# Kernel optimization log

Hardware: AMD Instinct MI355X
Metric: run time of the kernel (lower is better)

The kernel has to match this reference:

```python
import jax, jax.numpy as jnp
import numpy as np

B, T, H, CH = 8192, 10, 512, 512  # batch, time_step, hidden_size, code_hidden_size (must be equal)


def setup_inputs() -> dict:
    key = jax.random.key(0)
    ks = jax.random.split(key, 18)
    s = 0.05
    inp = {
        "h": jax.random.normal(ks[0], (B, T, CH), dtype=jnp.float32),
        "y_seq": jax.random.normal(ks[1], (B, T), dtype=jnp.float32),
        "attn1_w": jax.random.normal(ks[2], (CH, 2 * H), dtype=jnp.float32) * s,
        "attn1_b": jax.random.normal(ks[3], (CH,), dtype=jnp.float32) * s,
        "attn2_w": jax.random.normal(ks[4], (CH, CH), dtype=jnp.float32) * s,
        "attn2_b": jax.random.normal(ks[5], (CH,), dtype=jnp.float32) * s,
        "attn3_w": jax.random.normal(ks[6], (1, CH), dtype=jnp.float32) * s,
        "attn3_b": jax.random.normal(ks[7], (1,), dtype=jnp.float32) * s,
        "W_ih": jax.random.normal(ks[8], (4 * H, 1), dtype=jnp.float32) * s,
        "W_hh": jax.random.normal(ks[9], (4 * H, H), dtype=jnp.float32) * s,
        "b_ih": jax.random.normal(ks[10], (4 * H,), dtype=jnp.float32) * s,
        "b_hh": jax.random.normal(ks[11], (4 * H,), dtype=jnp.float32) * s,
        "fc1_w": jax.random.normal(ks[12], (H, CH + H), dtype=jnp.float32) * s,
        "fc1_b": jax.random.normal(ks[13], (H,), dtype=jnp.float32) * s,
        "fc2_w": jax.random.normal(ks[14], (1, H), dtype=jnp.float32) * s,
        "fc2_b": jax.random.normal(ks[15], (1,), dtype=jnp.float32) * s,
    }
    return inp


def reference(h, y_seq, attn1_w, attn1_b, attn2_w, attn2_b, attn3_w, attn3_b,
              W_ih, W_hh, b_ih, b_hh, fc1_w, fc1_b, fc2_w, fc2_b):
    # h: [B, T, CH] -> scan over time; y_seq: [B, T]
    h_t = jnp.transpose(h, (1, 0, 2))      # [T, B, CH]
    y_t = jnp.transpose(y_seq, (1, 0))     # [T, B]
    b = h.shape[0]
    hid = W_hh.shape[1]
    d0 = jnp.zeros((b, hid), dtype=h.dtype)
    s0 = jnp.zeros((b, hid), dtype=h.dtype)

    def step(carry, xs):
        d, s = carry
        ht, yt = xs  # ht: [B, CH], yt: [B]
        # attention scores (note: original softmax is over a singleton dim -> weights == 1)
        x = jnp.concatenate([d, ht], axis=1)                       # [B, 2H]
        a = jnp.tanh((x @ attn1_w.T + attn1_b) @ attn2_w.T + attn2_b)
        w = a @ attn3_w.T + attn3_b                                # [B, 1]
        w = jax.nn.softmax(w, axis=1)                              # softmax over size-1 dim == 1
        h1 = w * ht                                                # [B, H] (CH == H)
        # single LSTM step with h0 = h1, c0 = s, input = yt (scalar feature)
        gates = yt[:, None] @ W_ih.T + b_ih + h1 @ W_hh.T + b_hh   # [B, 4H]
        i, f, g, o = jnp.split(gates, 4, axis=1)
        c = jax.nn.sigmoid(f) * s + jax.nn.sigmoid(i) * jnp.tanh(g)
        d_new = jax.nn.sigmoid(o) * jnp.tanh(c)
        return (d_new, c), None

    (d, s), _ = jax.lax.scan(step, (d0, s0), (h_t, y_t))
    z = jnp.concatenate([d, h_t[-1]], axis=1)                      # [B, CH+H]
    y_res = (z @ fc1_w.T + fc1_b) @ fc2_w.T + fc2_b                # [B, 1]
    return y_res
```

## Files before the change

### kernel.cpp

```cpp
#include <hip/hip_runtime.h>
#include <stdint.h>

typedef __attribute__((ext_vector_type(8))) short short8;
typedef __attribute__((ext_vector_type(4))) float f32x4;
typedef unsigned short ushort_t;

#define T_STEPS 10
#define BT 128
#define WPACK_BYTES (2048*1024)
#define VBUF_OFF  WPACK_BYTES
#define HBF_OFF   (WPACK_BYTES + 8192)
#define H_ELEMS   (8192ull*T_STEPS*512)
#define HBF_BYTES (H_ELEMS*2)

typedef const __attribute__((address_space(1))) void gas_void;
typedef __attribute__((address_space(3))) void las_void;

__device__ __forceinline__ void gld_lds16(const void* g, void* l){
  __builtin_amdgcn_global_load_lds((gas_void*)g, (las_void*)l, 16, 0, 0);
}

__device__ __forceinline__ unsigned int pk2(float x, float y){
  unsigned int bx = __float_as_uint(x), by = __float_as_uint(y);
  bx = (bx + 0x7FFFu + ((bx>>16)&1u)) >> 16;
  by = (by + 0x7FFFu + ((by>>16)&1u)) >> 16;
  return bx | (by<<16);
}
__device__ __forceinline__ float sigf(float x){ return 1.f/(1.f + __expf(-x)); }
__device__ __forceinline__ float tanh_(float x){
  x = fminf(fmaxf(x, -15.f), 15.f);
  float e = __expf(2.f*x);
  return (e - 1.f)/(e + 1.f);
}

__global__ __launch_bounds__(256) void k_pack(const float* __restrict__ Whh,
                                              ushort_t* __restrict__ wp){
  int id  = blockIdx.x*256 + threadIdx.x;
  int row = id >> 6;
  int ko  = (id & 63) * 8;
  const float* p = Whh + row*512 + ko;
  float4 a = *(const float4*)p, b = *(const float4*)(p+4);
  uint4 v;
  v.x = pk2(a.x,a.y); v.y = pk2(a.z,a.w);
  v.z = pk2(b.x,b.y); v.w = pk2(b.z,b.w);
  int g = row >> 9, j = row & 511;
  int jb = j >> 6, jt = (j >> 4) & 3, jl = j & 15;
  int kc = ko >> 5, khi = (ko >> 3) & 3, lane = khi*16 + jl;
  int chunk = ((jb*4 + jt)*4 + g)*16 + kc;
  *(uint4*)(wp + chunk*512 + lane*8) = v;
}

__global__ __launch_bounds__(256) void k_v(const float* __restrict__ fc1w,
                                           const float* __restrict__ fc1b,
                                           const float* __restrict__ fc2w,
                                           const float* __restrict__ fc2b,
                                           float* __restrict__ vout,
                                           float* __restrict__ bias0){
  __shared__ float red[4][64];
  int tid = threadIdx.x;
  if (blockIdx.x < 16){
    int j  = blockIdx.x*64 + (tid & 63);
    int hc = tid >> 6;
    float s = 0.f;
    for (int hh = hc*128; hh < hc*128 + 128; ++hh)
      s += fc2w[hh] * fc1w[hh*1024 + j];
    red[hc][tid & 63] = s;
    __syncthreads();
    if (tid < 64)
      vout[blockIdx.x*64 + tid] = red[0][tid]+red[1][tid]+red[2][tid]+red[3][tid];
  } else {
    if (tid < 64){
      float s = 0.f;
      for (int i = 0; i < 8; ++i){ int hh = i*64 + tid; s += fc2w[hh]*fc1b[hh]; }
      for (int m = 32; m; m >>= 1) s += __shfl_xor(s, m);
      if (tid == 0) *bias0 = s + fc2b[0];
    }
  }
}

__global__ __launch_bounds__(512) void k_init(const float* __restrict__ h,
                                              const float* __restrict__ v,
                                              const float* __restrict__ bias0,
                                              float* __restrict__ out){
  int w = threadIdx.x >> 6, lane = threadIdx.x & 63;
  float b0v = *bias0;
  const float* v2 = v + 512;
  for (int r = 0; r < 8; ++r){
    int b = blockIdx.x*64 + w*8 + r;
    const float* hp = h + ((size_t)b*T_STEPS + 9)*512 + lane*8;
    float4 x0 = *(const float4*)hp, x1 = *(const float4*)(hp+4);
    const float* vp = v2 + lane*8;
    float4 w0 = *(const float4*)vp, w1 = *(const float4*)(vp+4);
    float s = x0.x*w0.x + x0.y*w0.y + x0.z*w0.z + x0.w*w0.w
            + x1.x*w1.x + x1.y*w1.y + x1.z*w1.z + x1.w*w1.w;
    for (int m = 32; m; m >>= 1) s += __shfl_xor(s, m);
    if (lane == 0) out[b] = s + b0v;
  }
}

__global__ __launch_bounds__(256) void k_prep(const float* __restrict__ h,
                                              ushort_t* __restrict__ hbf){
  __shared__ __align__(16) ushort_t buf[16*512*8];
  int T = blockIdx.x / T_STEPS, t = blockIdx.x % T_STEPS;
  int tid = threadIdx.x;
  int row = tid >> 1, half = tid & 1;
  const float* src = h + ((size_t)(T*128 + row)*T_STEPS + t)*512 + half*256;
#pragma unroll
  for (int g = 0; g < 32; ++g){
    int k0 = half*256 + g*8;
    float4 a = *(const float4*)(src + g*8);
    float4 b = *(const float4*)(src + g*8 + 4);
    uint4 pk;
    pk.x = pk2(a.x,a.y); pk.y = pk2(a.z,a.w);
    pk.z = pk2(b.x,b.y); pk.w = pk2(b.z,b.w);
    int kc = k0 >> 5, kq = (k0 >> 3) & 3;
    *(uint4*)&buf[(size_t)(kc*512 + kq*128 + row)*8] = pk;
  }
  __syncthreads();
  ushort_t* dst = hbf + ((size_t)(T*T_STEPS + t)*16)*4096;
#pragma unroll
  for (int i = 0; i < 32; ++i){
    int gr = tid + i*256;
    *(uint4*)(dst + gr*8) = *(const uint4*)&buf[gr*8];
  }
}

__global__ __launch_bounds__(256)
__attribute__((amdgpu_waves_per_eu(2, 2)))
void k_main_r(const ushort_t* __restrict__ hbf, const float* __restrict__ y,
              const float* __restrict__ Wih, const float* __restrict__ bih,
              const float* __restrict__ bhh,
              const ushort_t* __restrict__ wpack, const float* __restrict__ v1,
              float* __restrict__ out)
{
  __shared__ float ys[BT*T_STEPS];

  int tid = threadIdx.x;
  int w = tid >> 6, lane = tid & 63, lhi = lane >> 4, llo = lane & 15;
  int mh = w & 1, wj = w >> 1;
  int bid = blockIdx.x;
  int xcd = bid & 7, q = bid >> 3;
  int jb = q >> 3, tile = xcd*8 + (q & 7);
  int b0 = tile * BT;

  float bias2[4][2], wihv[4][2], v1v[2];
#pragma unroll
  for (int g = 0; g < 4; ++g)
#pragma unroll
    for (int n = 0; n < 2; ++n){
      int col = g*512 + jb*64 + (wj*2+n)*16 + llo;
      bias2[g][n] = bih[col] + bhh[col];
      wihv[g][n]  = Wih[col];
    }
#pragma unroll
  for (int n = 0; n < 2; ++n) v1v[n] = v1[jb*64 + (wj*2+n)*16 + llo];

  for (int i = tid; i < BT*T_STEPS; i += 256)
    ys[i] = y[(size_t)b0*T_STEPS + i];
  __syncthreads();

  const ushort_t* abase = hbf + (size_t)tile*655360
                        + (size_t)(lhi*128 + mh*64 + llo)*8;
  const ushort_t* wbase = wpack + (size_t)(jb*4 + wj*2)*32768 + lane*8;

  f32x4 acc[4][3][2];
  float cst[4][2][4];
#pragma unroll
  for (int m = 0; m < 4; ++m)
#pragma unroll
    for (int n = 0; n < 2; ++n){
#pragma unroll
      for (int g = 0; g < 3; ++g) acc[m][g][n] = (f32x4){0.f,0.f,0.f,0.f};
#pragma unroll
      for (int r = 0; r < 4; ++r) cst[m][n][r] = 0.f;
    }

  const ushort_t* aT = abase;
#pragma unroll 1
  for (int t = 0; t < T_STEPS; ++t){
    short8 afA[4], wfA[3][2], afB[4], wfB[3][2];
    const ushort_t* ap = aT;
    const ushort_t* wk = wbase;

#pragma unroll
    for (int m = 0; m < 4; ++m) afA[m] = *(const short8*)(ap + m*128);
#pragma unroll
    for (int g = 0; g < 3; ++g)
#pragma unroll
      for (int n = 0; n < 2; ++n)
        wfA[g][n] = *(const short8*)(wk + (size_t)(n*4+g)*8192);

#pragma unroll 1
    for (int kp = 0; kp < 8; ++kp){
#pragma unroll
      for (int m = 0; m < 4; ++m) afB[m] = *(const short8*)(ap + 4096 + m*128);
#pragma unroll
      for (int g = 0; g < 3; ++g)
#pragma unroll
        for (int n = 0; n < 2; ++n)
          wfB[g][n] = *(const short8*)(wk + (size_t)(n*4+g)*8192 + 512);
#pragma unroll
      for (int g = 0; g < 3; ++g)
#pragma unroll
        for (int n = 0; n < 2; ++n)
#pragma unroll
          for (int m = 0; m < 4; ++m)
            acc[m][g][n] = __builtin_amdgcn_mfma_f32_16x16x32_bf16(
                afA[m], wfA[g][n], acc[m][g][n], 0, 0, 0);
      if (kp < 7){
#pragma unroll
        for (int m = 0; m < 4; ++m) afA[m] = *(const short8*)(ap + 8192 + m*128);
#pragma unroll
        for (int g = 0; g < 3; ++g)
#pragma unroll
          for (int n = 0; n < 2; ++n)
            wfA[g][n] = *(const short8*)(wk + (size_t)(n*4+g)*8192 + 1024);
      }
#pragma unroll
      for (int g = 0; g < 3; ++g)
#pragma unroll
        for (int n = 0; n < 2; ++n)
#pragma unroll
          for (int m = 0; m < 4; ++m)
            acc[m][g][n] = __builtin_amdgcn_mfma_f32_16x16x32_bf16(
                afB[m], wfB[g][n], acc[m][g][n], 0, 0, 0);
      ap += 8192;
      wk += 1024;
    }

#pragma unroll
    for (int m = 0; m < 4; ++m)
#pragma unroll
      for (int r = 0; r < 4; ++r){
        float yr = ys[(mh*64 + m*16 + lhi*4 + r)*T_STEPS + t];
#pragma unroll
        for (int n = 0; n < 2; ++n){
          float pi = acc[m][0][n][r] + fmaf(yr, wihv[0][n], bias2[0][n]);
          float pf = acc[m][1][n][r] + fmaf(yr, wihv[1][n], bias2[1][n]);
          float pg = acc[m][2][n][r] + fmaf(yr, wihv[2][n], bias2[2][n]);
          cst[m][n][r] = sigf(pf)*cst[m][n][r] + sigf(pi)*tanh_(pg);
        }
      }
#pragma unroll
    for (int m = 0; m < 4; ++m)
#pragma unroll
      for (int g = 0; g < 3; ++g)
#pragma unroll
        for (int n = 0; n < 2; ++n) acc[m][g][n] = (f32x4){0.f,0.f,0.f,0.f};

    aT += 65536;
  }

  f32x4 acco[4][2];
#pragma unroll
  for (int m = 0; m < 4; ++m)
#pragma unroll
    for (int n = 0; n < 2; ++n) acco[m][n] = (f32x4){0.f,0.f,0.f,0.f};

  {
    const ushort_t* ap = abase + (size_t)9*65536;
    const ushort_t* wk = wbase + (size_t)3*8192;
    short8 afA[4], woA[2], afB[4], woB[2];
#pragma unroll
    for (int m = 0; m < 4; ++m) afA[m] = *(const short8*)(ap + m*128);
#pragma unroll
    for (int n = 0; n < 2; ++n) woA[n] = *(const short8*)(wk + (size_t)n*32768);

#pragma unroll 1
    for (int kp = 0; kp < 8; ++kp){
#pragma unroll
      for (int m = 0; m < 4; ++m) afB[m] = *(const short8*)(ap + 4096 + m*128);
#pragma unroll
      for (int n = 0; n < 2; ++n)
        woB[n] = *(const short8*)(wk + (size_t)n*32768 + 512);
#pragma unroll
      for (int n = 0; n < 2; ++n)
#pragma unroll
        for (int m = 0; m < 4; ++m)
          acco[m][n] = __builtin_amdgcn_mfma_f32_16x16x32_bf16(
              afA[m], woA[n], acco[m][n], 0, 0, 0);
      if (kp < 7){
#pragma unroll
        for (int m = 0; m < 4; ++m) afA[m] = *(const short8*)(ap + 8192 + m*128);
#pragma unroll
        for (int n = 0; n < 2; ++n)
          woA[n] = *(const short8*)(wk + (size_t)n*32768 + 1024);
      }
#pragma unroll
      for (int n = 0; n < 2; ++n)
#pragma unroll
        for (int m = 0; m < 4; ++m)
          acco[m][n] = __builtin_amdgcn_mfma_f32_16x16x32_bf16(
              afB[m], woB[n], acco[m][n], 0, 0, 0);
      ap += 8192;
      wk += 1024;
    }
  }

#pragma unroll
  for (int m = 0; m < 4; ++m)
#pragma unroll
    for (int r = 0; r < 4; ++r){
      float yr = ys[(mh*64 + m*16 + lhi*4 + r)*T_STEPS + 9];
      float val = 0.f;
#pragma unroll
      for (int n = 0; n < 2; ++n){
        float po = acco[m][n][r] + fmaf(yr, wihv[3][n], bias2[3][n]);
        val += sigf(po)*tanh_(cst[m][n][r])*v1v[n];
      }
      val += __shfl_xor(val, 1);
      val += __shfl_xor(val, 2);
      val += __shfl_xor(val, 4);
      val += __shfl_xor(val, 8);
      if (llo == 0)
        atomicAdd(&out[b0 + mh*64 + m*16 + lhi*4 + r], val);
    }
}

__global__ __launch_bounds__(256)
__attribute__((amdgpu_waves_per_eu(2, 2)))
void k_main_f(const float* __restrict__ h, const float* __restrict__ y,
              const float* __restrict__ Wih, const float* __restrict__ bih,
              const float* __restrict__ bhh,
              const ushort_t* __restrict__ wpack, const float* __restrict__ v1,
              float* __restrict__ out)
{
  __shared__ __align__(16) ushort_t Ab[2][4096];
  __shared__ float ys[BT*T_STEPS];

  int tid = threadIdx.x;
  int w = tid >> 6, lane = tid & 63, lhi = lane >> 4, llo = lane & 15;
  int mh = w & 1, wj = w >> 1;
  int bid = blockIdx.x;
  int xcd = bid & 7, q = bid >> 3;
  int jb = q >> 3, tile = xcd*8 + (q & 7);
  int b0 = tile * BT;

  float bias2[4][2], wihv[4][2], v1v[2];
#pragma unroll
  for (int g = 0; g < 4; ++g)
#pragma unroll
    for (int n = 0; n < 2; ++n){
      int col = g*512 + jb*64 + (wj*2+n)*16 + llo;
      bias2[g][n] = bih[col] + bhh[col];
      wihv[g][n]  = Wih[col];
    }
#pragma unroll
  for (int n = 0; n < 2; ++n) v1v[n] = v1[jb*64 + (wj*2+n)*16 + llo];

  for (int i = tid; i < BT*T_STEPS; i += 256)
    ys[i] = y[(size_t)b0*T_STEPS + i];

  const ushort_t* wbase = wpack + (size_t)(jb*4 + wj*2)*32768 + lane*8;

  auto stageA_f = [&](int parity, int ss){
    int t = (ss < 160) ? (ss >> 4) : 9;
    int kc = ss & 15;
#pragma unroll
    for (int i = 0; i < 2; ++i){
      int gidx = tid + i*256;
      int kq = gidx >> 7, row = gidx & 127;
      const float* p = h + ((size_t)(b0+row)*T_STEPS + t)*512 + kc*32 + kq*8;
      float4 x0 = *(const float4*)p, x1 = *(const float4*)(p+4);
      uint4 pk;
      pk.x = pk2(x0.x,x0.y); pk.y = pk2(x0.z,x0.w);
      pk.z = pk2(x1.x,x1.y); pk.w = pk2(x1.z,x1.w);
      *(uint4*)&Ab[parity][gidx*8] = pk;
    }
  };

  stageA_f(0, 0);
  __syncthreads();

  f32x4 acc[4][3][2];
  float cst[4][2][4];
#pragma unroll
  for (int m = 0; m < 4; ++m)
#pragma unroll
    for (int n = 0; n < 2; ++n){
#pragma unroll
      for (int g = 0; g < 3; ++g) acc[m][g][n] = (f32x4){0.f,0.f,0.f,0.f};
#pragma unroll
      for (int r = 0; r < 4; ++r) cst[m][n][r] = 0.f;
    }

  const int aro = (lhi*128 + mh*64 + llo)*8;

#pragma unroll 1
  for (int s = 0; s < 160; ++s){
    if (s < 159) stageA_f((s+1)&1, s+1);
    else         stageA_f(0, 160);

    int kco = (s & 15) * 512;
    short8 wf[3][2];
#pragma unroll
    for (int g = 0; g < 3; ++g)
#pragma unroll
      for (int n = 0; n < 2; ++n)
        wf[g][n] = *(const short8*)(wbase + (size_t)(n*4+g)*8192 + kco);

    const ushort_t* ap = &Ab[s&1][aro];
    short8 af[4];
#pragma unroll
    for (int m = 0; m < 4; ++m)
      af[m] = *(const short8*)(ap + m*128);

#pragma unroll
    for (int g = 0; g < 3; ++g)
#pragma unroll
      for (int n = 0; n < 2; ++n)
#pragma unroll
        for (int m = 0; m < 4; ++m)
          acc[m][g][n] = __builtin_amdgcn_mfma_f32_16x16x32_bf16(
              af[m], wf[g][n], acc[m][g][n], 0, 0, 0);

    if ((s & 15) == 15){
      int t = s >> 4;
#pragma unroll
      for (int m = 0; m < 4; ++m)
#pragma unroll
        for (int r = 0; r < 4; ++r){
          float yr = ys[(mh*64 + m*16 + lhi*4 + r)*T_STEPS + t];
#pragma unroll
          for (int n = 0; n < 2; ++n){
            float pi = acc[m][0][n][r] + fmaf(yr, wihv[0][n], bias2[0][n]);
            float pf = acc[m][1][n][r] + fmaf(yr, wihv[1][n], bias2[1][n]);
            float pg = acc[m][2][n][r] + fmaf(yr, wihv[2][n], bias2[2][n]);
            cst[m][n][r] = sigf(pf)*cst[m][n][r] + sigf(pi)*tanh_(pg);
          }
        }
#pragma unroll
      for (int m = 0; m < 4; ++m)
#pragma unroll
        for (int g = 0; g < 3; ++g)
#pragma unroll
          for (int n = 0; n < 2; ++n) acc[m][g][n] = (f32x4){0.f,0.f,0.f,0.f};
    }
    __syncthreads();
  }

  f32x4 acco[4][2];
#pragma unroll
  for (int m = 0; m < 4; ++m)
#pragma unroll
    for (int n = 0; n < 2; ++n) acco[m][n] = (f32x4){0.f,0.f,0.f,0.f};

#pragma unroll 1
  for (int s2 = 0; s2 < 16; ++s2){
    if (s2 < 15) stageA_f((s2+1)&1, 161+s2);
    int kco = s2 * 512;
    short8 wo[2];
#pragma unroll
    for (int n = 0; n < 2; ++n)
      wo[n] = *(const short8*)(wbase + (size_t)(n*4+3)*8192 + kco);

    const ushort_t* ap = &Ab[s2&1][aro];
    short8 af[4];
#pragma unroll
    for (int m = 0; m < 4; ++m)
      af[m] = *(const short8*)(ap + m*128);
#pragma unroll
    for (int n = 0; n < 2; ++n)
#pragma unroll
      for (int m = 0; m < 4; ++m)
        acco[m][n] = __builtin_amdgcn_mfma_f32_16x16x32_bf16(
            af[m], wo[n], acco[m][n], 0, 0, 0);
    __syncthreads();
  }

#pragma unroll
  for (int m = 0; m < 4; ++m)
#pragma unroll
    for (int r = 0; r < 4; ++r){
      float yr = ys[(mh*64 + m*16 + lhi*4 + r)*T_STEPS + 9];
      float val = 0.f;
#pragma unroll
      for (int n = 0; n < 2; ++n){
        float po = acco[m][n][r] + fmaf(yr, wihv[3][n], bias2[3][n]);
        val += sigf(po)*tanh_(cst[m][n][r])*v1v[n];
      }
      val += __shfl_xor(val, 1);
      val += __shfl_xor(val, 2);
      val += __shfl_xor(val, 4);
      val += __shfl_xor(val, 8);
      if (llo == 0)
        atomicAdd(&out[b0 + mh*64 + m*16 + lhi*4 + r], val);
    }
}

extern "C" void kernel_launch(void* const* d_in, const int* in_sizes, int n_in,
                              void* d_out, int out_size, void* d_ws, size_t ws_size,
                              hipStream_t stream){
  (void)in_sizes; (void)n_in; (void)out_size;
  const float* h    = (const float*)d_in[0];
  const float* y    = (const float*)d_in[1];
  const float* Wih  = (const float*)d_in[8];
  const float* Whh  = (const float*)d_in[9];
  const float* bih  = (const float*)d_in[10];
  const float* bhh  = (const float*)d_in[11];
  const float* fc1w = (const float*)d_in[12];
  const float* fc1b = (const float*)d_in[13];
  const float* fc2w = (const float*)d_in[14];
  const float* fc2b = (const float*)d_in[15];
  float* out = (float*)d_out;

  ushort_t* wpack = (ushort_t*)d_ws;
  float* vbuf  = (float*)((char*)d_ws + VBUF_OFF);
  float* bias0 = vbuf + 1024;
  ushort_t* hbf = (ushort_t*)((char*)d_ws + HBF_OFF);
  bool prep = ws_size >= (size_t)HBF_OFF + HBF_BYTES;

  k_pack<<<512, 256, 0, stream>>>(Whh, wpack);
  k_v<<<17, 256, 0, stream>>>(fc1w, fc1b, fc2w, fc2b, vbuf, bias0);
  if (prep)
    k_prep<<<64*T_STEPS, 256, 0, stream>>>(h, hbf);
  k_init<<<128, 512, 0, stream>>>(h, vbuf, bias0, out);
  if (prep)
    k_main_r<<<512, 256, 0, stream>>>(hbf, y, Wih, bih, bhh, wpack, vbuf, out);
  else
    k_main_f<<<512, 256, 0, stream>>>(h, y, Wih, bih, bhh, wpack, vbuf, out);
}
```

Measured before the change: 254.0 us.

## Stage hidden-state weights in LDS and pipeline A tiles with async loads

Replaces the register-direct main kernel with a version that keeps each block's slice of the packed W_hh gate weights resident in LDS. Each block now covers 256 batch rows by 32 hidden columns, so all four waves share the same weights. A tiles are streamed through double-buffered LDS using global_load_lds, with a software-pipelined register double buffer that fuses the ten time steps and the output-gate pass into one 176-step loop. The prep kernel's layout is changed to the 256-row tile format. The aim is to cut redundant global weight reads and improve reuse, at the cost of lower occupancy (one wave per EU) and more LDS.

```diff
diff --git a/kernel.cpp b/kernel.cpp
--- a/kernel.cpp
+++ b/kernel.cpp
@@ -6,7 +6,6 @@
 typedef unsigned short ushort_t;
 
 #define T_STEPS 10
-#define BT 128
 #define WPACK_BYTES (2048*1024)
 #define VBUF_OFF  WPACK_BYTES
 #define HBF_OFF   (WPACK_BYTES + 8192)
@@ -100,70 +99,96 @@
 
 __global__ __launch_bounds__(256) void k_prep(const float* __restrict__ h,
                                               ushort_t* __restrict__ hbf){
-  __shared__ __align__(16) ushort_t buf[16*512*8];
-  int T = blockIdx.x / T_STEPS, t = blockIdx.x % T_STEPS;
+  __shared__ __align__(16) ushort_t buf[8192*8];
+  int bid = blockIdx.x;
+  int T = bid / 20, rem = bid % 20, t = rem >> 1, half = rem & 1;
   int tid = threadIdx.x;
-  int row = tid >> 1, half = tid & 1;
-  const float* src = h + ((size_t)(T*128 + row)*T_STEPS + t)*512 + half*256;
+  int row128 = tid >> 1, khalf = tid & 1;
+  const float* src = h + ((size_t)(T*256 + half*128 + row128)*T_STEPS + t)*512
+                   + khalf*256;
 #pragma unroll
   for (int g = 0; g < 32; ++g){
-    int k0 = half*256 + g*8;
+    int k0 = khalf*256 + g*8;
     float4 a = *(const float4*)(src + g*8);
     float4 b = *(const float4*)(src + g*8 + 4);
     uint4 pk;
     pk.x = pk2(a.x,a.y); pk.y = pk2(a.z,a.w);
     pk.z = pk2(b.x,b.y); pk.w = pk2(b.z,b.w);
     int kc = k0 >> 5, kq = (k0 >> 3) & 3;
-    *(uint4*)&buf[(size_t)(kc*512 + kq*128 + row)*8] = pk;
+    *(uint4*)&buf[(size_t)(kc*512 + kq*128 + row128)*8] = pk;
   }
   __syncthreads();
-  ushort_t* dst = hbf + ((size_t)(T*T_STEPS + t)*16)*4096;
+  size_t sb = ((size_t)(T*T_STEPS + t)*16)*1024;
 #pragma unroll
   for (int i = 0; i < 32; ++i){
     int gr = tid + i*256;
-    *(uint4*)(dst + gr*8) = *(const uint4*)&buf[gr*8];
-  }
-}
+    int kc = gr >> 9, kq = (gr >> 7) & 3, r = gr & 127;
+    size_t dg = sb + (size_t)kc*1024 + kq*256 + half*128 + r;
+    *(uint4*)(hbf + dg*8) = *(const uint4*)&buf[gr*8];
+  }
+}
+
+struct RegSet { short8 af[4]; short8 wf[3][2]; };
 
 __global__ __launch_bounds__(256)
-__attribute__((amdgpu_waves_per_eu(2, 2)))
-void k_main_r(const ushort_t* __restrict__ hbf, const float* __restrict__ y,
+__attribute__((amdgpu_waves_per_eu(1, 1)))
+void k_main_p(const ushort_t* __restrict__ hbf, const float* __restrict__ y,
               const float* __restrict__ Wih, const float* __restrict__ bih,
               const float* __restrict__ bhh,
               const ushort_t* __restrict__ wpack, const float* __restrict__ v1,
               float* __restrict__ out)
 {
-  __shared__ float ys[BT*T_STEPS];
+  __shared__ __align__(16) ushort_t Wlds[96*512];
+  __shared__ __align__(16) ushort_t Ab[2][4][2048];
+  __shared__ float ys[256*T_STEPS];
 
   int tid = threadIdx.x;
   int w = tid >> 6, lane = tid & 63, lhi = lane >> 4, llo = lane & 15;
-  int mh = w & 1, wj = w >> 1;
   int bid = blockIdx.x;
   int xcd = bid & 7, q = bid >> 3;
-  int jb = q >> 3, tile = xcd*8 + (q & 7);
-  int b0 = tile * BT;
+  int jb  = q & 15;
+  int tile = xcd*2 + ((q >> 4) & 1) + ((q >> 5) << 4);
+  int b0 = tile * 256;
 
   float bias2[4][2], wihv[4][2], v1v[2];
 #pragma unroll
   for (int g = 0; g < 4; ++g)
 #pragma unroll
     for (int n = 0; n < 2; ++n){
-      int col = g*512 + jb*64 + (wj*2+n)*16 + llo;
+      int col = g*512 + jb*32 + n*16 + llo;
       bias2[g][n] = bih[col] + bhh[col];
       wihv[g][n]  = Wih[col];
     }
 #pragma unroll
-  for (int n = 0; n < 2; ++n) v1v[n] = v1[jb*64 + (wj*2+n)*16 + llo];
-
-  for (int i = tid; i < BT*T_STEPS; i += 256)
+  for (int n = 0; n < 2; ++n) v1v[n] = v1[jb*32 + n*16 + llo];
+
+  for (int i = tid; i < 256*T_STEPS; i += 256)
     ys[i] = y[(size_t)b0*T_STEPS + i];
-  __syncthreads();
-
-  const ushort_t* abase = hbf + (size_t)tile*655360
-                        + (size_t)(lhi*128 + mh*64 + llo)*8;
-  const ushort_t* wbase = wpack + (size_t)(jb*4 + wj*2)*32768 + lane*8;
+
+#pragma unroll
+  for (int i = 0; i < 24; ++i){
+    int c = w*24 + i;
+    int g = c >> 5, jt = (c >> 4) & 1, kc = c & 15;
+    int J = jb*2 + jt;
+    int ch = (((J >> 2)*4 + (J & 3))*4 + g)*16 + kc;
+    gld_lds16(wpack + (size_t)ch*512 + lane*8, Wlds + c*512);
+  }
+
+  const ushort_t* asrc = hbf + (size_t)tile*1310720 + (size_t)(w*64 + lane)*8;
+  {
+    ushort_t* dst = &Ab[0][w][0];
+    gld_lds16(asrc,        dst);
+    gld_lds16(asrc + 2048, dst + 512);
+    gld_lds16(asrc + 4096, dst + 1024);
+    gld_lds16(asrc + 6144, dst + 1536);
+    asrc += 8192;
+  }
+  asm volatile("s_waitcnt vmcnt(0) lgkmcnt(0)" ::: "memory");
+  __builtin_amdgcn_sched_barrier(0);
+  __builtin_amdgcn_s_barrier();
 
   f32x4 acc[4][3][2];
+  f32x4 acco[4][2];
   float cst[4][2][4];
 #pragma unroll
   for (int m = 0; m < 4; ++m)
@@ -171,34 +196,37 @@
     for (int n = 0; n < 2; ++n){
 #pragma unroll
       for (int g = 0; g < 3; ++g) acc[m][g][n] = (f32x4){0.f,0.f,0.f,0.f};
+      acco[m][n] = (f32x4){0.f,0.f,0.f,0.f};
 #pragma unroll
       for (int r = 0; r < 4; ++r) cst[m][n][r] = 0.f;
     }
 
-  const ushort_t* aT = abase;
-#pragma unroll 1
-  for (int t = 0; t < T_STEPS; ++t){
-    short8 afA[4], wfA[3][2], afB[4], wfB[3][2];
-    const ushort_t* ap = aT;
-    const ushort_t* wk = wbase;
-
-#pragma unroll
-    for (int m = 0; m < 4; ++m) afA[m] = *(const short8*)(ap + m*128);
+  RegSet sA, sB;
+  const int aoff = (lhi*64 + llo)*8;
+  {
+    const ushort_t* ar = &Ab[0][w][aoff];
+#pragma unroll
+    for (int m = 0; m < 4; ++m) sA.af[m] = *(const short8*)(ar + m*128);
 #pragma unroll
     for (int g = 0; g < 3; ++g)
 #pragma unroll
       for (int n = 0; n < 2; ++n)
-        wfA[g][n] = *(const short8*)(wk + (size_t)(n*4+g)*8192);
-
-#pragma unroll 1
-    for (int kp = 0; kp < 8; ++kp){
-#pragma unroll
-      for (int m = 0; m < 4; ++m) afB[m] = *(const short8*)(ap + 4096 + m*128);
-#pragma unroll
-      for (int g = 0; g < 3; ++g)
-#pragma unroll
-        for (int n = 0; n < 2; ++n)
-          wfB[g][n] = *(const short8*)(wk + (size_t)(n*4+g)*8192 + 512);
+        sA.wf[g][n] = *(const short8*)(Wlds + ((g*2+n)*16 + 0)*512 + lane*8);
+  }
+
+  auto body = [&](int ss, RegSet& cur, RegSet& nxt){
+    int ns = ss + 1;
+    if (ns < 176){
+      if (ns == 160) asrc -= 131072;
+      ushort_t* dst = &Ab[ns & 1][w][0];
+      gld_lds16(asrc,        dst);
+      gld_lds16(asrc + 2048, dst + 512);
+      gld_lds16(asrc + 4096, dst + 1024);
+      gld_lds16(asrc + 6144, dst + 1536);
+      asrc += 8192;
+    }
+    int kc = ss & 15;
+    if (ss < 160){
 #pragma unroll
       for (int g = 0; g < 3; ++g)
 #pragma unroll
@@ -206,102 +234,72 @@
 #pragma unroll
           for (int m = 0; m < 4; ++m)
             acc[m][g][n] = __builtin_amdgcn_mfma_f32_16x16x32_bf16(
-                afA[m], wfA[g][n], acc[m][g][n], 0, 0, 0);
-      if (kp < 7){
-#pragma unroll
-        for (int m = 0; m < 4; ++m) afA[m] = *(const short8*)(ap + 8192 + m*128);
-#pragma unroll
-        for (int g = 0; g < 3; ++g)
-#pragma unroll
-          for (int n = 0; n < 2; ++n)
-            wfA[g][n] = *(const short8*)(wk + (size_t)(n*4+g)*8192 + 1024);
+                cur.af[m], cur.wf[g][n], acc[m][g][n], 0, 0, 0);
+      if (kc == 15){
+        int t = ss >> 4;
+#pragma unroll
+        for (int m = 0; m < 4; ++m)
+#pragma unroll
+          for (int r = 0; r < 4; ++r){
+            float yr = ys[(w*64 + m*16 + lhi*4 + r)*T_STEPS + t];
+#pragma unroll
+            for (int n = 0; n < 2; ++n){
+              float pi = acc[m][0][n][r] + fmaf(yr, wihv[0][n], bias2[0][n]);
+              float pf = acc[m][1][n][r] + fmaf(yr, wihv[1][n], bias2[1][n]);
+              float pg = acc[m][2][n][r] + fmaf(yr, wihv[2][n], bias2[2][n]);
+              cst[m][n][r] = sigf(pf)*cst[m][n][r] + sigf(pi)*tanh_(pg);
+            }
+          }
+#pragma unroll
+        for (int m = 0; m < 4; ++m)
+#pragma unroll
+          for (int g = 0; g < 3; ++g)
+#pragma unroll
+            for (int n = 0; n < 2; ++n) acc[m][g][n] = (f32x4){0.f,0.f,0.f,0.f};
       }
-#pragma unroll
-      for (int g = 0; g < 3; ++g)
-#pragma unroll
-        for (int n = 0; n < 2; ++n)
-#pragma unroll
-          for (int m = 0; m < 4; ++m)
-            acc[m][g][n] = __builtin_amdgcn_mfma_f32_16x16x32_bf16(
-                afB[m], wfB[g][n], acc[m][g][n], 0, 0, 0);
-      ap += 8192;
-      wk += 1024;
-    }
-
-#pragma unroll
-    for (int m = 0; m < 4; ++m)
-#pragma unroll
-      for (int r = 0; r < 4; ++r){
-        float yr = ys[(mh*64 + m*16 + lhi*4 + r)*T_STEPS + t];
-#pragma unroll
-        for (int n = 0; n < 2; ++n){
-          float pi = acc[m][0][n][r] + fmaf(yr, wihv[0][n], bias2[0][n]);
-          float pf = acc[m][1][n][r] + fmaf(yr, wihv[1][n], bias2[1][n]);
-          float pg = acc[m][2][n][r] + fmaf(yr, wihv[2][n], bias2[2][n]);
-          cst[m][n][r] = sigf(pf)*cst[m][n][r] + sigf(pi)*tanh_(pg);
-        }
+    } else {
+      short8 wo[2];
+#pragma unroll
+      for (int n = 0; n < 2; ++n){
+        int J = jb*2 + n;
+        int ch = (((J >> 2)*4 + (J & 3))*4 + 3)*16 + kc;
+        wo[n] = *(const short8*)(wpack + (size_t)ch*512 + lane*8);
       }
-#pragma unroll
-    for (int m = 0; m < 4; ++m)
-#pragma unroll
-      for (int g = 0; g < 3; ++g)
-#pragma unroll
-        for (int n = 0; n < 2; ++n) acc[m][g][n] = (f32x4){0.f,0.f,0.f,0.f};
-
-    aT += 65536;
-  }
-
-  f32x4 acco[4][2];
-#pragma unroll
-  for (int m = 0; m < 4; ++m)
-#pragma unroll
-    for (int n = 0; n < 2; ++n) acco[m][n] = (f32x4){0.f,0.f,0.f,0.f};
-
-  {
-    const ushort_t* ap = abase + (size_t)9*65536;
-    const ushort_t* wk = wbase + (size_t)3*8192;
-    short8 afA[4], woA[2], afB[4], woB[2];
-#pragma unroll
-    for (int m = 0; m < 4; ++m) afA[m] = *(const short8*)(ap + m*128);
-#pragma unroll
-    for (int n = 0; n < 2; ++n) woA[n] = *(const short8*)(wk + (size_t)n*32768);
-
-#pragma unroll 1
-    for (int kp = 0; kp < 8; ++kp){
-#pragma unroll
-      for (int m = 0; m < 4; ++m) afB[m] = *(const short8*)(ap + 4096 + m*128);
-#pragma unroll
-      for (int n = 0; n < 2; ++n)
-        woB[n] = *(const short8*)(wk + (size_t)n*32768 + 512);
 #pragma unroll
       for (int n = 0; n < 2; ++n)
 #pragma unroll
         for (int m = 0; m < 4; ++m)
           acco[m][n] = __builtin_amdgcn_mfma_f32_16x16x32_bf16(
-              afA[m], woA[n], acco[m][n], 0, 0, 0);
-      if (kp < 7){
-#pragma unroll
-        for (int m = 0; m < 4; ++m) afA[m] = *(const short8*)(ap + 8192 + m*128);
-#pragma unroll
-        for (int n = 0; n < 2; ++n)
-          woA[n] = *(const short8*)(wk + (size_t)n*32768 + 1024);
+              cur.af[m], wo[n], acco[m][n], 0, 0, 0);
+    }
+    if (ns < 176){
+      asm volatile("s_waitcnt vmcnt(0)" ::: "memory");
+      __builtin_amdgcn_sched_barrier(0);
+      const ushort_t* ar = &Ab[ns & 1][w][aoff];
+#pragma unroll
+      for (int m = 0; m < 4; ++m) nxt.af[m] = *(const short8*)(ar + m*128);
+      if (ns < 160){
+        int nkc = ns & 15;
+#pragma unroll
+        for (int g = 0; g < 3; ++g)
+#pragma unroll
+          for (int n = 0; n < 2; ++n)
+            nxt.wf[g][n] = *(const short8*)(Wlds + ((g*2+n)*16 + nkc)*512 + lane*8);
       }
-#pragma unroll
-      for (int n = 0; n < 2; ++n)
-#pragma unroll
-        for (int m = 0; m < 4; ++m)
-          acco[m][n] = __builtin_amdgcn_mfma_f32_16x16x32_bf16(
-              afB[m], woB[n], acco[m][n], 0, 0, 0);
-      ap += 8192;
-      wk += 1024;
-    }
+    }
+  };
+
+#pragma unroll 1
+  for (int i = 0; i < 88; ++i){
+    body(2*i,     sA, sB);
+    body(2*i + 1, sB, sA);
   }
 
 #pragma unroll
   for (int m = 0; m < 4; ++m)
 #pragma unroll
     for (int r = 0; r < 4; ++r){
-      float yr = ys[(mh*64 + m*16 + lhi*4 + r)*T_STEPS + 9];
+      float yr = ys[(w*64 + m*16 + lhi*4 + r)*T_STEPS + 9];
       float val = 0.f;
 #pragma unroll
       for (int n = 0; n < 2; ++n){
@@ -313,7 +311,7 @@
       val += __shfl_xor(val, 4);
       val += __shfl_xor(val, 8);
       if (llo == 0)
-        atomicAdd(&out[b0 + mh*64 + m*16 + lhi*4 + r], val);
+        atomicAdd(&out[b0 + w*64 + m*16 + lhi*4 + r], val);
     }
 }
 
@@ -325,8 +323,8 @@
               const ushort_t* __restrict__ wpack, const float* __restrict__ v1,
               float* __restrict__ out)
 {
-  __shared__ __align__(16) ushort_t Ab[2][4096];
-  __shared__ float ys[BT*T_STEPS];
+  __shared__ __align__(16) ushort_t Abf[2][4096];
+  __shared__ float ysf[128*T_STEPS];
 
   int tid = threadIdx.x;
   int w = tid >> 6, lane = tid & 63, lhi = lane >> 4, llo = lane & 15;
@@ -334,7 +332,7 @@
   int bid = blockIdx.x;
   int xcd = bid & 7, q = bid >> 3;
   int jb = q >> 3, tile = xcd*8 + (q & 7);
-  int b0 = tile * BT;
+  int b0 = tile * 128;
 
   float bias2[4][2], wihv[4][2], v1v[2];
 #pragma unroll
@@ -348,8 +346,8 @@
 #pragma unroll
   for (int n = 0; n < 2; ++n) v1v[n] = v1[jb*64 + (wj*2+n)*16 + llo];
 
-  for (int i = tid; i < BT*T_STEPS; i += 256)
-    ys[i] = y[(size_t)b0*T_STEPS + i];
+  for (int i = tid; i < 128*T_STEPS; i += 256)
+    ysf[i] = y[(size_t)b0*T_STEPS + i];
 
   const ushort_t* wbase = wpack + (size_t)(jb*4 + wj*2)*32768 + lane*8;
 
@@ -365,7 +363,7 @@
       uint4 pk;
       pk.x = pk2(x0.x,x0.y); pk.y = pk2(x0.z,x0.w);
       pk.z = pk2(x1.x,x1.y); pk.w = pk2(x1.z,x1.w);
-      *(uint4*)&Ab[parity][gidx*8] = pk;
+      *(uint4*)&Abf[parity][gidx*8] = pk;
     }
   };
 
@@ -399,7 +397,7 @@
       for (int n = 0; n < 2; ++n)
         wf[g][n] = *(const short8*)(wbase + (size_t)(n*4+g)*8192 + kco);
 
-    const ushort_t* ap = &Ab[s&1][aro];
+    const ushort_t* ap = &Abf[s&1][aro];
     short8 af[4];
 #pragma unroll
     for (int m = 0; m < 4; ++m)
@@ -420,7 +418,7 @@
       for (int m = 0; m < 4; ++m)
 #pragma unroll
         for (int r = 0; r < 4; ++r){
-          float yr = ys[(mh*64 + m*16 + lhi*4 + r)*T_STEPS + t];
+          float yr = ysf[(mh*64 + m*16 + lhi*4 + r)*T_STEPS + t];
 #pragma unroll
           for (int n = 0; n < 2; ++n){
             float pi = acc[m][0][n][r] + fmaf(yr, wihv[0][n], bias2[0][n]);
@@ -454,7 +452,7 @@
     for (int n = 0; n < 2; ++n)
       wo[n] = *(const short8*)(wbase + (size_t)(n*4+3)*8192 + kco);
 
-    const ushort_t* ap = &Ab[s2&1][aro];
+    const ushort_t* ap = &Abf[s2&1][aro];
     short8 af[4];
 #pragma unroll
     for (int m = 0; m < 4; ++m)
@@ -472,7 +470,7 @@
   for (int m = 0; m < 4; ++m)
 #pragma unroll
     for (int r = 0; r < 4; ++r){
-      float yr = ys[(mh*64 + m*16 + lhi*4 + r)*T_STEPS + 9];
+      float yr = ysf[(mh*64 + m*16 + lhi*4 + r)*T_STEPS + 9];
       float val = 0.f;
 #pragma unroll
       for (int n = 0; n < 2; ++n){
@@ -513,10 +511,10 @@
   k_pack<<<512, 256, 0, stream>>>(Whh, wpack);
   k_v<<<17, 256, 0, stream>>>(fc1w, fc1b, fc2w, fc2b, vbuf, bias0);
   if (prep)
-    k_prep<<<64*T_STEPS, 256, 0, stream>>>(h, hbf);
+    k_prep<<<640, 256, 0, stream>>>(h, hbf);
   k_init<<<128, 512, 0, stream>>>(h, vbuf, bias0, out);
   if (prep)
-    k_main_r<<<512, 256, 0, stream>>>(hbf, y, Wih, bih, bhh, wpack, vbuf, out);
+    k_main_p<<<512, 256, 0, stream>>>(hbf, y, Wih, bih, bhh, wpack, vbuf, out);
   else
     k_main_f<<<512, 256, 0, stream>>>(h, y, Wih, bih, bhh, wpack, vbuf, out);
 }
```

After: 420.1 us. +65.4%, slower.

## Stage W_hh slice in LDS and retile main kernel to 256-row batch tiles

Applied to the files above, without the earlier changes.

The main kernel now uses 512-thread blocks covering 256 batch rows by 32 hidden columns. Each block loads its 96 chunks of packed W_hh (i,f,g gates) into LDS once via global_load_lds and reuses them across all time steps, instead of streaming weights from global memory every step. The prep kernel now lays out the bf16 h tiles in 256-row groups to match. This trades a large LDS allocation (96 KB), which limits occupancy, for lower global/L2 weight traffic. Each wave now works on a narrower M dimension, so MFMA work per fragment load changes.

```diff
diff --git a/kernel.cpp b/kernel.cpp
--- a/kernel.cpp
+++ b/kernel.cpp
@@ -6,7 +6,6 @@
 typedef unsigned short ushort_t;
 
 #define T_STEPS 10
-#define BT 128
 #define WPACK_BYTES (2048*1024)
 #define VBUF_OFF  WPACK_BYTES
 #define HBF_OFF   (WPACK_BYTES + 8192)
@@ -100,73 +99,86 @@
 
 __global__ __launch_bounds__(256) void k_prep(const float* __restrict__ h,
                                               ushort_t* __restrict__ hbf){
-  __shared__ __align__(16) ushort_t buf[16*512*8];
-  int T = blockIdx.x / T_STEPS, t = blockIdx.x % T_STEPS;
+  __shared__ __align__(16) ushort_t buf[8192*8];
+  int bid = blockIdx.x;
+  int T = bid / 20, rem = bid % 20, t = rem >> 1, half = rem & 1;
   int tid = threadIdx.x;
-  int row = tid >> 1, half = tid & 1;
-  const float* src = h + ((size_t)(T*128 + row)*T_STEPS + t)*512 + half*256;
+  int row128 = tid >> 1, khalf = tid & 1;
+  const float* src = h + ((size_t)(T*256 + half*128 + row128)*T_STEPS + t)*512
+                   + khalf*256;
 #pragma unroll
   for (int g = 0; g < 32; ++g){
-    int k0 = half*256 + g*8;
+    int k0 = khalf*256 + g*8;
     float4 a = *(const float4*)(src + g*8);
     float4 b = *(const float4*)(src + g*8 + 4);
     uint4 pk;
     pk.x = pk2(a.x,a.y); pk.y = pk2(a.z,a.w);
     pk.z = pk2(b.x,b.y); pk.w = pk2(b.z,b.w);
     int kc = k0 >> 5, kq = (k0 >> 3) & 3;
-    *(uint4*)&buf[(size_t)(kc*512 + kq*128 + row)*8] = pk;
+    *(uint4*)&buf[(size_t)(kc*512 + kq*128 + row128)*8] = pk;
   }
   __syncthreads();
-  ushort_t* dst = hbf + ((size_t)(T*T_STEPS + t)*16)*4096;
+  size_t sb = ((size_t)(T*T_STEPS + t)*16)*1024;
 #pragma unroll
   for (int i = 0; i < 32; ++i){
     int gr = tid + i*256;
-    *(uint4*)(dst + gr*8) = *(const uint4*)&buf[gr*8];
-  }
-}
-
-__global__ __launch_bounds__(256)
+    int kc = gr >> 9, kq = (gr >> 7) & 3, r = gr & 127;
+    size_t dg = sb + (size_t)kc*1024 + kq*256 + half*128 + r;
+    *(uint4*)(hbf + dg*8) = *(const uint4*)&buf[gr*8];
+  }
+}
+
+__global__ __launch_bounds__(512)
 __attribute__((amdgpu_waves_per_eu(2, 2)))
-void k_main_r(const ushort_t* __restrict__ hbf, const float* __restrict__ y,
+void k_main_p(const ushort_t* __restrict__ hbf, const float* __restrict__ y,
               const float* __restrict__ Wih, const float* __restrict__ bih,
               const float* __restrict__ bhh,
               const ushort_t* __restrict__ wpack, const float* __restrict__ v1,
               float* __restrict__ out)
 {
-  __shared__ float ys[BT*T_STEPS];
+  __shared__ __align__(16) ushort_t Wlds[96*512];
+  __shared__ float ys[256*T_STEPS];
 
   int tid = threadIdx.x;
   int w = tid >> 6, lane = tid & 63, lhi = lane >> 4, llo = lane & 15;
-  int mh = w & 1, wj = w >> 1;
   int bid = blockIdx.x;
   int xcd = bid & 7, q = bid >> 3;
-  int jb = q >> 3, tile = xcd*8 + (q & 7);
-  int b0 = tile * BT;
+  int jb  = q & 15;
+  int tile = xcd*4 + (q >> 4);
+  int b0 = tile * 256;
 
   float bias2[4][2], wihv[4][2], v1v[2];
 #pragma unroll
   for (int g = 0; g < 4; ++g)
 #pragma unroll
     for (int n = 0; n < 2; ++n){
-      int col = g*512 + jb*64 + (wj*2+n)*16 + llo;
+      int col = g*512 + jb*32 + n*16 + llo;
       bias2[g][n] = bih[col] + bhh[col];
       wihv[g][n]  = Wih[col];
     }
 #pragma unroll
-  for (int n = 0; n < 2; ++n) v1v[n] = v1[jb*64 + (wj*2+n)*16 + llo];
-
-  for (int i = tid; i < BT*T_STEPS; i += 256)
+  for (int n = 0; n < 2; ++n) v1v[n] = v1[jb*32 + n*16 + llo];
+
+  for (int i = tid; i < 256*T_STEPS; i += 512)
     ys[i] = y[(size_t)b0*T_STEPS + i];
+
+#pragma unroll
+  for (int i = 0; i < 12; ++i){
+    int c = w*12 + i;
+    int g = c >> 5, n = (c >> 4) & 1, kc = c & 15;
+    int ch = (((jb >> 1)*4 + ((jb & 1)*2 + n))*4 + g)*16 + kc;
+    gld_lds16(wpack + (size_t)ch*512 + lane*8, Wlds + c*512);
+  }
   __syncthreads();
 
-  const ushort_t* abase = hbf + (size_t)tile*655360
-                        + (size_t)(lhi*128 + mh*64 + llo)*8;
-  const ushort_t* wbase = wpack + (size_t)(jb*4 + wj*2)*32768 + lane*8;
-
-  f32x4 acc[4][3][2];
-  float cst[4][2][4];
-#pragma unroll
-  for (int m = 0; m < 4; ++m)
+  const ushort_t* wl = Wlds + lane*8;
+  const ushort_t* aT = hbf + (size_t)tile*1310720
+                     + (size_t)(lhi*256 + w*32 + llo)*8;
+
+  f32x4 acc[2][3][2];
+  float cst[2][2][4];
+#pragma unroll
+  for (int m = 0; m < 2; ++m)
 #pragma unroll
     for (int n = 0; n < 2; ++n){
 #pragma unroll
@@ -175,64 +187,62 @@
       for (int r = 0; r < 4; ++r) cst[m][n][r] = 0.f;
     }
 
-  const ushort_t* aT = abase;
 #pragma unroll 1
   for (int t = 0; t < T_STEPS; ++t){
-    short8 afA[4], wfA[3][2], afB[4], wfB[3][2];
     const ushort_t* ap = aT;
-    const ushort_t* wk = wbase;
-
-#pragma unroll
-    for (int m = 0; m < 4; ++m) afA[m] = *(const short8*)(ap + m*128);
+    short8 afA[2], wfA[3][2], afB[2], wfB[3][2];
+#pragma unroll
+    for (int m = 0; m < 2; ++m) afA[m] = *(const short8*)(ap + m*128);
 #pragma unroll
     for (int g = 0; g < 3; ++g)
 #pragma unroll
       for (int n = 0; n < 2; ++n)
-        wfA[g][n] = *(const short8*)(wk + (size_t)(n*4+g)*8192);
+        wfA[g][n] = *(const short8*)(wl + (g*2+n)*8192);
 
 #pragma unroll 1
     for (int kp = 0; kp < 8; ++kp){
-#pragma unroll
-      for (int m = 0; m < 4; ++m) afB[m] = *(const short8*)(ap + 4096 + m*128);
+      const ushort_t* wk1 = wl + (2*kp + 1)*512;
+#pragma unroll
+      for (int m = 0; m < 2; ++m) afB[m] = *(const short8*)(ap + 8192 + m*128);
 #pragma unroll
       for (int g = 0; g < 3; ++g)
 #pragma unroll
         for (int n = 0; n < 2; ++n)
-          wfB[g][n] = *(const short8*)(wk + (size_t)(n*4+g)*8192 + 512);
+          wfB[g][n] = *(const short8*)(wk1 + (g*2+n)*8192);
 #pragma unroll
       for (int g = 0; g < 3; ++g)
 #pragma unroll
         for (int n = 0; n < 2; ++n)
 #pragma unroll
-          for (int m = 0; m < 4; ++m)
+          for (int m = 0; m < 2; ++m)
             acc[m][g][n] = __builtin_amdgcn_mfma_f32_16x16x32_bf16(
                 afA[m], wfA[g][n], acc[m][g][n], 0, 0, 0);
       if (kp < 7){
-#pragma unroll
-        for (int m = 0; m < 4; ++m) afA[m] = *(const short8*)(ap + 8192 + m*128);
+        const ushort_t* wk2 = wl + (2*kp + 2)*512;
+#pragma unroll
+        for (int m = 0; m < 2; ++m) afA[m] = *(const short8*)(ap + 16384 + m*128);
 #pragma unroll
         for (int g = 0; g < 3; ++g)
 #pragma unroll
           for (int n = 0; n < 2; ++n)
-            wfA[g][n] = *(const short8*)(wk + (size_t)(n*4+g)*8192 + 1024);
+            wfA[g][n] = *(const short8*)(wk2 + (g*2+n)*8192);
       }
 #pragma unroll
       for (int g = 0; g < 3; ++g)
 #pragma unroll
         for (int n = 0; n < 2; ++n)
 #pragma unroll
-          for (int m = 0; m < 4; ++m)
+          for (int m = 0; m < 2; ++m)
             acc[m][g][n] = __builtin_amdgcn_mfma_f32_16x16x32_bf16(
                 afB[m], wfB[g][n], acc[m][g][n], 0, 0, 0);
-      ap += 8192;
-      wk += 1024;
-    }
-
-#pragma unroll
-    for (int m = 0; m < 4; ++m)
+      ap += 16384;
+    }
+
+#pragma unroll
+    for (int m = 0; m < 2; ++m)
 #pragma unroll
       for (int r = 0; r < 4; ++r){
-        float yr = ys[(mh*64 + m*16 + lhi*4 + r)*T_STEPS + t];
+        float yr = ys[(w*32 + m*16 + lhi*4 + r)*T_STEPS + t];
 #pragma unroll
         for (int n = 0; n < 2; ++n){
           float pi = acc[m][0][n][r] + fmaf(yr, wihv[0][n], bias2[0][n]);
@@ -242,66 +252,64 @@
         }
       }
 #pragma unroll
-    for (int m = 0; m < 4; ++m)
+    for (int m = 0; m < 2; ++m)
 #pragma unroll
       for (int g = 0; g < 3; ++g)
 #pragma unroll
         for (int n = 0; n < 2; ++n) acc[m][g][n] = (f32x4){0.f,0.f,0.f,0.f};
 
-    aT += 65536;
-  }
-
-  f32x4 acco[4][2];
-#pragma unroll
-  for (int m = 0; m < 4; ++m)
+    aT += 131072;
+  }
+
+  f32x4 acco[2][2];
+#pragma unroll
+  for (int m = 0; m < 2; ++m)
 #pragma unroll
     for (int n = 0; n < 2; ++n) acco[m][n] = (f32x4){0.f,0.f,0.f,0.f};
 
   {
-    const ushort_t* ap = abase + (size_t)9*65536;
-    const ushort_t* wk = wbase + (size_t)3*8192;
-    short8 afA[4], woA[2], afB[4], woB[2];
-#pragma unroll
-    for (int m = 0; m < 4; ++m) afA[m] = *(const short8*)(ap + m*128);
-#pragma unroll
-    for (int n = 0; n < 2; ++n) woA[n] = *(const short8*)(wk + (size_t)n*32768);
+    const ushort_t* ap = aT - 131072;
+    const ushort_t* wo0 = wpack + (size_t)((((jb>>1)*4 + (jb&1)*2 + 0)*4 + 3)*16)*512 + lane*8;
+    const ushort_t* wo1 = wpack + (size_t)((((jb>>1)*4 + (jb&1)*2 + 1)*4 + 3)*16)*512 + lane*8;
+    short8 afA[2], woA[2], afB[2], woB[2];
+#pragma unroll
+    for (int m = 0; m < 2; ++m) afA[m] = *(const short8*)(ap + m*128);
+    woA[0] = *(const short8*)(wo0);
+    woA[1] = *(const short8*)(wo1);
 
 #pragma unroll 1
     for (int kp = 0; kp < 8; ++kp){
 #pragma unroll
-      for (int m = 0; m < 4; ++m) afB[m] = *(const short8*)(ap + 4096 + m*128);
+      for (int m = 0; m < 2; ++m) afB[m] = *(const short8*)(ap + 8192 + m*128);
+      woB[0] = *(const short8*)(wo0 + (2*kp+1)*512);
+      woB[1] = *(const short8*)(wo1 + (2*kp+1)*512);
 #pragma unroll
       for (int n = 0; n < 2; ++n)
-        woB[n] = *(const short8*)(wk + (size_t)n*32768 + 512);
-#pragma unroll
-      for (int n = 0; n < 2; ++n)
-#pragma unroll
-        for (int m = 0; m < 4; ++m)
+#pragma unroll
+        for (int m = 0; m < 2; ++m)
           acco[m][n] = __builtin_amdgcn_mfma_f32_16x16x32_bf16(
               afA[m], woA[n], acco[m][n], 0, 0, 0);
       if (kp < 7){
 #pragma unroll
-        for (int m = 0; m < 4; ++m) afA[m] = *(const short8*)(ap + 8192 + m*128);
-#pragma unroll
-        for (int n = 0; n < 2; ++n)
-          woA[n] = *(const short8*)(wk + (size_t)n*32768 + 1024);
+        for (int m = 0; m < 2; ++m) afA[m] = *(const short8*)(ap + 16384 + m*128);
+        woA[0] = *(const short8*)(wo0 + (2*kp+2)*512);
+        woA[1] = *(const short8*)(wo1 + (2*kp+2)*512);
       }
 #pragma unroll
       for (int n = 0; n < 2; ++n)
 #pragma unroll
-        for (int m = 0; m < 4; ++m)
+        for (int m = 0; m < 2; ++m)
           acco[m][n] = __builtin_amdgcn_mfma_f32_16x16x32_bf16(
               afB[m], woB[n], acco[m][n], 0, 0, 0);
-      ap += 8192;
-      wk += 1024;
-    }
-  }
-
-#pragma unroll
-  for (int m = 0; m < 4; ++m)
+      ap += 16384;
+    }
+  }
+
+#pragma unroll
+  for (int m = 0; m < 2; ++m)
 #pragma unroll
     for (int r = 0; r < 4; ++r){
-      float yr = ys[(mh*64 + m*16 + lhi*4 + r)*T_STEPS + 9];
+      float yr = ys[(w*32 + m*16 + lhi*4 + r)*T_STEPS + 9];
       float val = 0.f;
 #pragma unroll
       for (int n = 0; n < 2; ++n){
@@ -313,7 +321,7 @@
       val += __shfl_xor(val, 4);
       val += __shfl_xor(val, 8);
       if (llo == 0)
-        atomicAdd(&out[b0 + mh*64 + m*16 + lhi*4 + r], val);
+        atomicAdd(&out[b0 + w*32 + m*16 + lhi*4 + r], val);
     }
 }
 
@@ -325,8 +333,8 @@
               const ushort_t* __restrict__ wpack, const float* __restrict__ v1,
               float* __restrict__ out)
 {
-  __shared__ __align__(16) ushort_t Ab[2][4096];
-  __shared__ float ys[BT*T_STEPS];
+  __shared__ __align__(16) ushort_t Abf[2][4096];
+  __shared__ float ysf[128*T_STEPS];
 
   int tid = threadIdx.x;
   int w = tid >> 6, lane = tid & 63, lhi = lane >> 4, llo = lane & 15;
@@ -334,7 +342,7 @@
   int bid = blockIdx.x;
   int xcd = bid & 7, q = bid >> 3;
   int jb = q >> 3, tile = xcd*8 + (q & 7);
-  int b0 = tile * BT;
+  int b0 = tile * 128;
 
   float bias2[4][2], wihv[4][2], v1v[2];
 #pragma unroll
@@ -348,8 +356,8 @@
 #pragma unroll
   for (int n = 0; n < 2; ++n) v1v[n] = v1[jb*64 + (wj*2+n)*16 + llo];
 
-  for (int i = tid; i < BT*T_STEPS; i += 256)
-    ys[i] = y[(size_t)b0*T_STEPS + i];
+  for (int i = tid; i < 128*T_STEPS; i += 256)
+    ysf[i] = y[(size_t)b0*T_STEPS + i];
 
   const ushort_t* wbase = wpack + (size_t)(jb*4 + wj*2)*32768 + lane*8;
 
@@ -365,7 +373,7 @@
       uint4 pk;
       pk.x = pk2(x0.x,x0.y); pk.y = pk2(x0.z,x0.w);
       pk.z = pk2(x1.x,x1.y); pk.w = pk2(x1.z,x1.w);
-      *(uint4*)&Ab[parity][gidx*8] = pk;
+      *(uint4*)&Abf[parity][gidx*8] = pk;
     }
   };
 
@@ -399,7 +407,7 @@
       for (int n = 0; n < 2; ++n)
         wf[g][n] = *(const short8*)(wbase + (size_t)(n*4+g)*8192 + kco);
 
-    const ushort_t* ap = &Ab[s&1][aro];
+    const ushort_t* ap = &Abf[s&1][aro];
     short8 af[4];
 #pragma unroll
     for (int m = 0; m < 4; ++m)
@@ -420,7 +428,7 @@
       for (int m = 0; m < 4; ++m)
 #pragma unroll
         for (int r = 0; r < 4; ++r){
-          float yr = ys[(mh*64 + m*16 + lhi*4 + r)*T_STEPS + t];
+          float yr = ysf[(mh*64 + m*16 + lhi*4 + r)*T_STEPS + t];
 #pragma unroll
           for (int n = 0; n < 2; ++n){
             float pi = acc[m][0][n][r] + fmaf(yr, wihv[0][n], bias2[0][n]);
@@ -454,7 +462,7 @@
     for (int n = 0; n < 2; ++n)
       wo[n] = *(const short8*)(wbase + (size_t)(n*4+3)*8192 + kco);
 
-    const ushort_t* ap = &Ab[s2&1][aro];
+    const ushort_t* ap = &Abf[s2&1][aro];
     short8 af[4];
 #pragma unroll
     for (int m = 0; m < 4; ++m)
@@ -472,7 +480,7 @@
   for (int m = 0; m < 4; ++m)
 #pragma unroll
     for (int r = 0; r < 4; ++r){
-      float yr = ys[(mh*64 + m*16 + lhi*4 + r)*T_STEPS + 9];
+      float yr = ysf[(mh*64 + m*16 + lhi*4 + r)*T_STEPS + 9];
       float val = 0.f;
 #pragma unroll
       for (int n = 0; n < 2; ++n){
@@ -513,10 +521,10 @@
   k_pack<<<512, 256, 0, stream>>>(Whh, wpack);
   k_v<<<17, 256, 0, stream>>>(fc1w, fc1b, fc2w, fc2b, vbuf, bias0);
   if (prep)
-    k_prep<<<64*T_STEPS, 256, 0, stream>>>(h, hbf);
+    k_prep<<<640, 256, 0, stream>>>(h, hbf);
   k_init<<<128, 512, 0, stream>>>(h, vbuf, bias0, out);
   if (prep)
-    k_main_r<<<512, 256, 0, stream>>>(hbf, y, Wih, bih, bhh, wpack, vbuf, out);
+    k_main_p<<<512, 512, 0, stream>>>(hbf, y, Wih, bih, bhh, wpack, vbuf, out);
   else
     k_main_f<<<512, 256, 0, stream>>>(h, y, Wih, bih, bhh, wpack, vbuf, out);
 }
```

Result: faster. 231.4 us (median of 2 runs) (-8.9%).
